# Performance work log

Hardware: AMD Instinct MI355X
Metric: run time of the kernel (lower is better)

The kernel has to match this reference:

```python
import jax, jax.numpy as jnp
import numpy as np
from jax import lax

B, T, I, H, C = 64, 512, 512, 1024, 1000


def _lstm_layer(x, W_ih, W_hh, b_ih, b_hh):
    # x: [B, T, in]; W_ih: [4H, in]; W_hh: [4H, H]; biases: [4H]
    # Precompute input projections for all timesteps (one big GEMM).
    xW = jnp.einsum('bti,gi->btg', x, W_ih) + b_ih + b_hh  # [B, T, 4H]
    h0 = jnp.zeros((x.shape[0], W_hh.shape[1]), x.dtype)
    c0 = jnp.zeros_like(h0)

    def step(carry, xw_t):
        h, c = carry
        gates = xw_t + h @ W_hh.T  # [B, 4H]
        i, f, g, o = jnp.split(gates, 4, axis=-1)  # PyTorch gate order i,f,g,o
        i = jax.nn.sigmoid(i)
        f = jax.nn.sigmoid(f)
        g = jnp.tanh(g)
        o = jax.nn.sigmoid(o)
        c = f * c + i * g
        h = o * jnp.tanh(c)
        return (h, c), h

    (h_T, c_T), hs = lax.scan(step, (h0, c0), jnp.swapaxes(xW, 0, 1))
    return jnp.swapaxes(hs, 0, 1), h_T  # [B, T, H], [B, H]


def setup_inputs() -> dict:
    key = jax.random.key(0)
    ks = jax.random.split(key, 11)
    s_i = 1.0 / np.sqrt(H)
    u = lambda k, shape: jax.random.uniform(k, shape, jnp.float32, -s_i, s_i)
    return {
        'x': jax.random.normal(ks[0], (B, T, I), jnp.float32),
        'W_ih0': u(ks[1], (4 * H, I)),
        'W_hh0': u(ks[2], (4 * H, H)),
        'b_ih0': u(ks[3], (4 * H,)),
        'b_hh0': u(ks[4], (4 * H,)),
        'W_ih1': u(ks[5], (4 * H, H)),
        'W_hh1': u(ks[6], (4 * H, H)),
        'b_ih1': u(ks[7], (4 * H,)),
        'b_hh1': u(ks[8], (4 * H,)),
        'W_d': u(ks[9], (C, H)),
        'b_d': u(ks[10], (C,)),
    }


def reference(x, W_ih0, W_hh0, b_ih0, b_hh0, W_ih1, W_hh1, b_ih1, b_hh1, W_d, b_d):
    h1_seq, _ = _lstm_layer(x, W_ih0, W_hh0, b_ih0, b_hh0)
    _, h_last = _lstm_layer(h1_seq, W_ih1, W_hh1, b_ih1, b_hh1)
    return h_last @ W_d.T + b_d  # [B, num_classes]
```

## Files before the change

### kernel.cpp

```cpp
#include <hip/hip_runtime.h>

typedef short short8 __attribute__((ext_vector_type(8)));
typedef float f32x4 __attribute__((ext_vector_type(4)));
typedef int i32x4 __attribute__((ext_vector_type(4)));
typedef unsigned short u16;
typedef unsigned long long u64;

#define NBLK 256
#define BDIM 512
#define BB 64
#define TT 512
#define II 512
#define HH 1024
#define NCLS 1000
#define HBUF (BB*HH)

__device__ __forceinline__ u16 f2bf(float f) {
  union { float f; unsigned u; } v; v.f = f;
  unsigned u = v.u;
  u += 0x7fffu + ((u >> 16) & 1u);
  return (u16)(u >> 16);
}

__device__ __forceinline__ short8 cvt8(f32x4 a, f32x4 b) {
  short8 v;
  v[0] = (short)f2bf(a[0]); v[1] = (short)f2bf(a[1]);
  v[2] = (short)f2bf(a[2]); v[3] = (short)f2bf(a[3]);
  v[4] = (short)f2bf(b[0]); v[5] = (short)f2bf(b[1]);
  v[6] = (short)f2bf(b[2]); v[7] = (short)f2bf(b[3]);
  return v;
}

__device__ __forceinline__ unsigned ld_rlx(const unsigned* p) {
  return __hip_atomic_load(p, __ATOMIC_RELAXED, __HIP_MEMORY_SCOPE_AGENT);
}
__device__ __forceinline__ void st_rlx(unsigned* p, unsigned v) {
  __hip_atomic_store(p, v, __ATOMIC_RELAXED, __HIP_MEMORY_SCOPE_AGENT);
}

__global__ void cvt_x(const float* __restrict__ x, u16* __restrict__ xb, int n8) {
  int i = blockIdx.x * blockDim.x + threadIdx.x;
  const int stride = gridDim.x * blockDim.x;
  for (; i < n8; i += stride) {
    f32x4 a = ((const f32x4*)x)[2 * i];
    f32x4 b = ((const f32x4*)x)[2 * i + 1];
    ((short8*)xb)[i] = cvt8(a, b);
  }
}

template<bool XBF>
__global__ __launch_bounds__(BDIM, 2) void lstm2_fused(
    const float* __restrict__ x, const u16* __restrict__ xb,
    const float* __restrict__ Wih0, const float* __restrict__ Whh0,
    const float* __restrict__ bih0, const float* __restrict__ bhh0,
    const float* __restrict__ Wih1, const float* __restrict__ Whh1,
    const float* __restrict__ bih1, const float* __restrict__ bhh1,
    u16* __restrict__ ring,
    u16* __restrict__ h1buf,
    float* __restrict__ h1f,
    unsigned* __restrict__ bar)
{
  __shared__ u16 wlds[32 * 2048];
  __shared__ float gbuf[64][33];
  __shared__ float blds[32];

  const bool isL1 = (blockIdx.x >= 128);
  const int wgl = isL1 ? (int)blockIdx.x - 128 : (int)blockIdx.x;
  const int j0 = wgl * 8;
  const int KX = isL1 ? HH : II;
  const int RL = KX + HH;
  const int ROWB = RL * 2;
  const float* Wih = isL1 ? Wih1 : Wih0;
  const float* Whh = isL1 ? Whh1 : Whh0;

  {
    const int cpr = RL / 8;
    for (int idx = threadIdx.x; idx < 32 * cpr; idx += BDIM) {
      int n = idx / cpr, cb = idx - n * cpr;
      int r = ((n >> 3) << 10) + j0 + (n & 7);
      int k = cb * 8;
      const float* src = (k < KX) ? (Wih + (size_t)r * KX + k)
                                  : (Whh + (size_t)r * HH + (k - KX));
      f32x4 a = *(const f32x4*)src;
      f32x4 b = *(const f32x4*)(src + 4);
      short8 v = cvt8(a, b);
      unsigned byte = (unsigned)(n * ROWB + k * 2) ^ ((unsigned)(n & 7) << 4);
      *(short8*)((char*)wlds + byte) = v;
    }
    if (threadIdx.x < 32) {
      int n = threadIdx.x;
      int r = ((n >> 3) << 10) + j0 + (n & 7);
      blds[n] = (isL1 ? bih1[r] : bih0[r]) + (isL1 ? bhh1[r] : bhh0[r]);
    }
  }
  __syncthreads();

  const int lane = threadIdx.x & 63;
  const int wid = threadIdx.x >> 6;
  const int mt = wid & 3, kg = wid >> 2;
  const int m0 = mt << 4;
  const int row_a = m0 + (lane & 15);
  const int koff = (lane >> 4) << 3;
  const unsigned mask = (unsigned)(lane & 7) << 4;
  const unsigned nb0 = (unsigned)((lane & 15) * ROWB);
  const unsigned nb1 = nb0 + (unsigned)(16 * ROWB);
  const char* wch = (const char*)wlds;

  const int tb = threadIdx.x >> 3, tj = threadIdx.x & 7;

  const int nsteps = RL >> 5;
  const int half = nsteps >> 1;
  const int ks_begin = kg * half, ks_end = ks_begin + half;
  const int bstep = KX >> 5;
  const int r1e = (ks_end < bstep) ? ks_end : bstep;
  const int r2b = (ks_begin > bstep) ? ks_begin : bstep;

  unsigned* const arrA = bar;
  unsigned* const relA = bar + 64;
  unsigned* const arrB = bar + 256;
  unsigned* const relB = bar + 320;

  float c_state = 0.f;

  auto kloop_h = [&](const u16* base, int kadj, int ks0, int ks1,
                     f32x4& A0, f32x4& A1) {
    for (int c = ks0; c < ks1; c += 8) {
      i32x4 av[8];
#pragma unroll
      for (int i = 0; i < 8; ++i) {
        const u16* p = base + (((c + i) << 5) + koff - kadj);
        asm volatile("global_load_dwordx4 %0, %1, off sc0 sc1"
                     : "=v"(av[i]) : "v"(p));
      }
      asm volatile("s_waitcnt vmcnt(0)" ::: "memory");
      __builtin_amdgcn_sched_barrier(0);
#pragma unroll
      for (int i = 0; i < 8; ++i) {
        int kk = ((c + i) << 5) + koff;
        unsigned o = (unsigned)(kk * 2) ^ mask;
        short8 bv0 = *(const short8*)(wch + (nb0 + o));
        short8 bv1 = *(const short8*)(wch + (nb1 + o));
        union { i32x4 q; short8 s; } u; u.q = av[i];
        A0 = __builtin_amdgcn_mfma_f32_16x16x32_bf16(u.s, bv0, A0, 0, 0, 0);
        A1 = __builtin_amdgcn_mfma_f32_16x16x32_bf16(u.s, bv1, A1, 0, 0, 0);
      }
    }
  };

  auto step_tail = [&](f32x4 acc0, f32x4 acc1, u16* hout, bool wf) {
    const int colA = lane & 15;
    const int rowD = m0 + ((lane >> 4) << 2);
    if (kg == 1) {
#pragma unroll
      for (int r = 0; r < 4; ++r) {
        gbuf[rowD + r][colA] = acc0[r];
        gbuf[rowD + r][colA + 16] = acc1[r];
      }
    }
    __syncthreads();
    if (kg == 0) {
#pragma unroll
      for (int r = 0; r < 4; ++r) {
        gbuf[rowD + r][colA] += acc0[r];
        gbuf[rowD + r][colA + 16] += acc1[r];
      }
    }
    __syncthreads();
    float gi = gbuf[tb][tj]      + blds[tj];
    float gf = gbuf[tb][8 + tj]  + blds[8 + tj];
    float gg = gbuf[tb][16 + tj] + blds[16 + tj];
    float go = gbuf[tb][24 + tj] + blds[24 + tj];
    gi = 1.f / (1.f + __expf(-gi));
    gf = 1.f / (1.f + __expf(-gf));
    go = 1.f / (1.f + __expf(-go));
    float e2 = __expf(2.f * fminf(15.f, fmaxf(-15.f, gg)));
    gg = (e2 - 1.f) / (e2 + 1.f);
    c_state = gf * c_state + gi * gg;
    float e2c = __expf(2.f * fminf(15.f, fmaxf(-15.f, c_state)));
    float th = (e2c - 1.f) / (e2c + 1.f);
    float hval = go * th;
    unsigned hu = (unsigned)f2bf(hval);
    unsigned nbv = (unsigned)__shfl_xor((int)hu, 1);
    if ((tj & 1) == 0) {
      unsigned packed = hu | (nbv << 16);
      unsigned* dst = (unsigned*)(hout + (size_t)tb * HH + j0 + tj);
      st_rlx(dst, packed);
    }
    if (wf) h1f[(size_t)tb * HH + j0 + tj] = hval;
  };

  if (!isL1) {
    for (int t = 0; t < TT; ++t) {
      if (t >= 3) {
        if (threadIdx.x == 0)
          while (ld_rlx(relB) < (unsigned)(t - 2)) __builtin_amdgcn_s_sleep(2);
        __syncthreads();
      }
      f32x4 acc0 = {0,0,0,0}, acc1 = {0,0,0,0};
      if (XBF) {
        const u16* xr = xb + (size_t)t * II + (size_t)row_a * ((size_t)TT * II);
#pragma unroll
        for (int ks = ks_begin; ks < r1e; ++ks) {
          int kk = (ks << 5) + koff;
          short8 av = *(const short8*)(xr + kk);
          unsigned o = (unsigned)(kk * 2) ^ mask;
          short8 bv0 = *(const short8*)(wch + (nb0 + o));
          short8 bv1 = *(const short8*)(wch + (nb1 + o));
          acc0 = __builtin_amdgcn_mfma_f32_16x16x32_bf16(av, bv0, acc0, 0, 0, 0);
          acc1 = __builtin_amdgcn_mfma_f32_16x16x32_bf16(av, bv1, acc1, 0, 0, 0);
        }
      } else {
        const float* xr = x + (size_t)t * II + (size_t)row_a * ((size_t)TT * II);
#pragma unroll
        for (int ks = ks_begin; ks < r1e; ++ks) {
          int kk = (ks << 5) + koff;
          short8 av = cvt8(*(const f32x4*)(xr + kk), *(const f32x4*)(xr + kk + 4));
          unsigned o = (unsigned)(kk * 2) ^ mask;
          short8 bv0 = *(const short8*)(wch + (nb0 + o));
          short8 bv1 = *(const short8*)(wch + (nb1 + o));
          acc0 = __builtin_amdgcn_mfma_f32_16x16x32_bf16(av, bv0, acc0, 0, 0, 0);
          acc1 = __builtin_amdgcn_mfma_f32_16x16x32_bf16(av, bv1, acc1, 0, 0, 0);
        }
      }
      kloop_h(ring + (size_t)((t + 2) % 3) * HBUF + (size_t)row_a * HH, KX,
              r2b, ks_end, acc0, acc1);
      step_tail(acc0, acc1, ring + (size_t)(t % 3) * HBUF, false);
      __syncthreads();
      if (threadIdx.x == 0) {
        unsigned old = atomicAdd(arrA, 1u);
        if (old == (unsigned)(128 * (t + 1) - 1)) st_rlx(relA, (unsigned)(t + 1));
        else if (t < TT - 1)
          while (ld_rlx(relA) < (unsigned)(t + 1)) __builtin_amdgcn_s_sleep(2);
      }
      __syncthreads();
    }
  } else {
    for (int t = 0; t < TT; ++t) {
      if (threadIdx.x == 0)
        while (ld_rlx(relA) < (unsigned)(t + 1)) __builtin_amdgcn_s_sleep(2);
      __syncthreads();
      f32x4 acc0 = {0,0,0,0}, acc1 = {0,0,0,0};
      kloop_h(ring + (size_t)(t % 3) * HBUF + (size_t)row_a * HH, 0,
              ks_begin, r1e, acc0, acc1);
      kloop_h(h1buf + (size_t)((t + 1) & 1) * HBUF + (size_t)row_a * HH, KX,
              r2b, ks_end, acc0, acc1);
      step_tail(acc0, acc1, h1buf + (size_t)(t & 1) * HBUF, t == TT - 1);
      if (t < TT - 1) {
        __syncthreads();
        if (threadIdx.x == 0) {
          unsigned old = atomicAdd(arrB, 1u);
          if (old == (unsigned)(128 * (t + 1) - 1)) st_rlx(relB, (unsigned)(t + 1));
          else
            while (ld_rlx(relB) < (unsigned)(t + 1)) __builtin_amdgcn_s_sleep(2);
        }
        __syncthreads();
      }
    }
  }
}

__global__ void dense_out(const float* __restrict__ h1, const float* __restrict__ Wd,
                          const float* __restrict__ bd, float* __restrict__ out)
{
  const int b  = threadIdx.x & 63;
  const int cl = threadIdx.x >> 6;
  const int cc = blockIdx.x * 4 + cl;
  float acc = 0.f;
  const float* hrow = h1 + (size_t)b * HH;
  const float* wrow = Wd + (size_t)cc * HH;
#pragma unroll 8
  for (int k = 0; k < HH; k += 4) {
    f32x4 hv = *(const f32x4*)(hrow + k);
    f32x4 wv = *(const f32x4*)(wrow + k);
    acc += hv[0] * wv[0] + hv[1] * wv[1] + hv[2] * wv[2] + hv[3] * wv[3];
  }
  out[(size_t)b * NCLS + cc] = acc + bd[cc];
}

extern "C" void kernel_launch(void* const* d_in, const int* in_sizes, int n_in,
                              void* d_out, int out_size, void* d_ws, size_t ws_size,
                              hipStream_t stream)
{
  (void)in_sizes; (void)n_in; (void)out_size;
  const float* x    = (const float*)d_in[0];
  const float* Wih0 = (const float*)d_in[1];
  const float* Whh0 = (const float*)d_in[2];
  const float* bih0 = (const float*)d_in[3];
  const float* bhh0 = (const float*)d_in[4];
  const float* Wih1 = (const float*)d_in[5];
  const float* Whh1 = (const float*)d_in[6];
  const float* bih1 = (const float*)d_in[7];
  const float* bhh1 = (const float*)d_in[8];
  const float* Wd   = (const float*)d_in[9];
  const float* bd   = (const float*)d_in[10];

  unsigned* bar = (unsigned*)d_ws;
  float* h1f  = (float*)((char*)d_ws + 4096);
  u16* h1buf  = (u16*)((char*)d_ws + 272 * 1024);
  u16* ring   = (u16*)((char*)d_ws + 528 * 1024);
  u16* xb     = (u16*)((char*)d_ws + (1u << 20));

  const size_t needA = (1u << 20) + (size_t)BB * TT * II * 2;
  const bool tierA = (ws_size >= needA);

  hipMemsetAsync(d_ws, 0, 912 * 1024, stream);

  if (tierA) {
    hipLaunchKernelGGL(cvt_x, dim3(2048), dim3(256), 0, stream,
                       x, xb, (int)((size_t)BB * TT * II / 8));
    hipLaunchKernelGGL((lstm2_fused<true>), dim3(NBLK), dim3(BDIM), 0, stream,
                       x, xb, Wih0, Whh0, bih0, bhh0, Wih1, Whh1, bih1, bhh1,
                       ring, h1buf, h1f, bar);
  } else {
    hipLaunchKernelGGL((lstm2_fused<false>), dim3(NBLK), dim3(BDIM), 0, stream,
                       x, xb, Wih0, Whh0, bih0, bhh0, Wih1, Whh1, bih1, bhh1,
                       ring, h1buf, h1f, bar);
  }
  hipLaunchKernelGGL(dense_out, dim3(250), dim3(256), 0, stream, h1f, Wd, bd,
                     (float*)d_out);
}
```

Measured before the change: 5.418 ms.

## Hold LSTM weights in registers and use 32x32 MFMA with 4-way K split

Each wave now preloads its slice of the recurrent and input weights from LDS into registers once, before the time loop, instead of re-reading them from LDS every step. The 16x16x32 MFMAs split two ways over K are replaced by 32x32x16 MFMAs split four ways over K, with each wave owning a 32-row batch half. The gate reduction now sums four partial buffers stored in the otherwise unused tail of the weight LDS region, which removes one barrier. This raises register pressure considerably (24 to 32 short8 values per lane) under launch bounds of 2 blocks, which may cause spills.

New measurement: 5.521 ms. Within noise of the previous version (+1.9%).

```diff
diff --git a/kernel.cpp b/kernel.cpp
--- a/kernel.cpp
+++ b/kernel.cpp
@@ -2,6 +2,7 @@
 
 typedef short short8 __attribute__((ext_vector_type(8)));
 typedef float f32x4 __attribute__((ext_vector_type(4)));
+typedef float f32x16 __attribute__((ext_vector_type(16)));
 typedef int i32x4 __attribute__((ext_vector_type(4)));
 typedef unsigned short u16;
 typedef unsigned long long u64;
@@ -45,6 +46,51 @@
     f32x4 a = ((const f32x4*)x)[2 * i];
     f32x4 b = ((const f32x4*)x)[2 * i + 1];
     ((short8*)xb)[i] = cvt8(a, b);
+  }
+}
+
+
+template<int N, int B0, int MH>
+__device__ __forceinline__ void run_coh(const u16* lanep,
+                                        const short8 (&breg)[MH], f32x16& acc) {
+  static_assert(N % 8 == 0, "");
+#pragma unroll
+  for (int c = 0; c < N; c += 8) {
+    i32x4 av[8];
+#pragma unroll
+    for (int i = 0; i < 8; ++i) {
+      const u16* p = lanep + (c + i) * 16;
+      asm volatile("global_load_dwordx4 %0, %1, off sc0 sc1"
+                   : "=v"(av[i]) : "v"(p));
+    }
+    asm volatile("s_waitcnt vmcnt(0)" ::: "memory");
+    __builtin_amdgcn_sched_barrier(0);
+#pragma unroll
+    for (int i = 0; i < 8; ++i) {
+      union { i32x4 q; short8 s; } u; u.q = av[i];
+      acc = __builtin_amdgcn_mfma_f32_32x32x16_bf16(u.s, breg[B0 + c + i], acc, 0, 0, 0);
+    }
+  }
+}
+
+template<int N, int B0, int MH>
+__device__ __forceinline__ void run_pb(const u16* lanep,
+                                       const short8 (&breg)[MH], f32x16& acc) {
+#pragma unroll
+  for (int i = 0; i < N; ++i) {
+    short8 av = *(const short8*)(lanep + i * 16);
+    acc = __builtin_amdgcn_mfma_f32_32x32x16_bf16(av, breg[B0 + i], acc, 0, 0, 0);
+  }
+}
+
+template<int N, int B0, int MH>
+__device__ __forceinline__ void run_pf(const float* lanep,
+                                       const short8 (&breg)[MH], f32x16& acc) {
+#pragma unroll
+  for (int i = 0; i < N; ++i) {
+    short8 av = cvt8(*(const f32x4*)(lanep + i * 16),
+                     *(const f32x4*)(lanep + i * 16 + 4));
+    acc = __builtin_amdgcn_mfma_f32_32x32x16_bf16(av, breg[B0 + i], acc, 0, 0, 0);
   }
 }
 
@@ -61,8 +107,8 @@
     unsigned* __restrict__ bar)
 {
   __shared__ u16 wlds[32 * 2048];
-  __shared__ float gbuf[64][33];
   __shared__ float blds[32];
+  float (*g4)[64][32] = (float(*)[64][32])((char*)wlds + 98304);
 
   const bool isL1 = (blockIdx.x >= 128);
   const int wgl = isL1 ? (int)blockIdx.x - 128 : (int)blockIdx.x;
@@ -97,23 +143,12 @@
 
   const int lane = threadIdx.x & 63;
   const int wid = threadIdx.x >> 6;
-  const int mt = wid & 3, kg = wid >> 2;
-  const int m0 = mt << 4;
-  const int row_a = m0 + (lane & 15);
-  const int koff = (lane >> 4) << 3;
-  const unsigned mask = (unsigned)(lane & 7) << 4;
-  const unsigned nb0 = (unsigned)((lane & 15) * ROWB);
-  const unsigned nb1 = nb0 + (unsigned)(16 * ROWB);
+  const int mp = wid & 1, kq = wid >> 1;
+  const int row_a = mp * 32 + (lane & 31);
+  const int sub8 = (lane >> 5) << 3;
   const char* wch = (const char*)wlds;
 
   const int tb = threadIdx.x >> 3, tj = threadIdx.x & 7;
-
-  const int nsteps = RL >> 5;
-  const int half = nsteps >> 1;
-  const int ks_begin = kg * half, ks_end = ks_begin + half;
-  const int bstep = KX >> 5;
-  const int r1e = (ks_end < bstep) ? ks_end : bstep;
-  const int r2b = (ks_begin > bstep) ? ks_begin : bstep;
 
   unsigned* const arrA = bar;
   unsigned* const relA = bar + 64;
@@ -122,59 +157,25 @@
 
   float c_state = 0.f;
 
-  auto kloop_h = [&](const u16* base, int kadj, int ks0, int ks1,
-                     f32x4& A0, f32x4& A1) {
-    for (int c = ks0; c < ks1; c += 8) {
-      i32x4 av[8];
-#pragma unroll
-      for (int i = 0; i < 8; ++i) {
-        const u16* p = base + (((c + i) << 5) + koff - kadj);
-        asm volatile("global_load_dwordx4 %0, %1, off sc0 sc1"
-                     : "=v"(av[i]) : "v"(p));
-      }
-      asm volatile("s_waitcnt vmcnt(0)" ::: "memory");
-      __builtin_amdgcn_sched_barrier(0);
-#pragma unroll
-      for (int i = 0; i < 8; ++i) {
-        int kk = ((c + i) << 5) + koff;
-        unsigned o = (unsigned)(kk * 2) ^ mask;
-        short8 bv0 = *(const short8*)(wch + (nb0 + o));
-        short8 bv1 = *(const short8*)(wch + (nb1 + o));
-        union { i32x4 q; short8 s; } u; u.q = av[i];
-        A0 = __builtin_amdgcn_mfma_f32_16x16x32_bf16(u.s, bv0, A0, 0, 0, 0);
-        A1 = __builtin_amdgcn_mfma_f32_16x16x32_bf16(u.s, bv1, A1, 0, 0, 0);
-      }
-    }
-  };
-
-  auto step_tail = [&](f32x4 acc0, f32x4 acc1, u16* hout, bool wf) {
-    const int colA = lane & 15;
-    const int rowD = m0 + ((lane >> 4) << 2);
-    if (kg == 1) {
-#pragma unroll
-      for (int r = 0; r < 4; ++r) {
-        gbuf[rowD + r][colA] = acc0[r];
-        gbuf[rowD + r][colA + 16] = acc1[r];
-      }
+  auto step_tail = [&](const f32x16& acc, u16* hout, bool wf) {
+    const int col = lane & 31;
+    const int rbase = mp * 32 + ((lane >> 5) << 2);
+#pragma unroll
+    for (int r = 0; r < 16; ++r) {
+      int brow = rbase + (r & 3) + ((r >> 2) << 3);
+      g4[kq][brow][col] = acc[r];
     }
     __syncthreads();
-    if (kg == 0) {
-#pragma unroll
-      for (int r = 0; r < 4; ++r) {
-        gbuf[rowD + r][colA] += acc0[r];
-        gbuf[rowD + r][colA + 16] += acc1[r];
-      }
-    }
-    __syncthreads();
-    float gi = gbuf[tb][tj]      + blds[tj];
-    float gf = gbuf[tb][8 + tj]  + blds[8 + tj];
-    float gg = gbuf[tb][16 + tj] + blds[16 + tj];
-    float go = gbuf[tb][24 + tj] + blds[24 + tj];
-    gi = 1.f / (1.f + __expf(-gi));
-    gf = 1.f / (1.f + __expf(-gf));
-    go = 1.f / (1.f + __expf(-go));
-    float e2 = __expf(2.f * fminf(15.f, fmaxf(-15.f, gg)));
-    gg = (e2 - 1.f) / (e2 + 1.f);
+    float gv[4];
+#pragma unroll
+    for (int g = 0; g < 4; ++g)
+      gv[g] = g4[0][tb][g * 8 + tj] + g4[1][tb][g * 8 + tj]
+            + g4[2][tb][g * 8 + tj] + g4[3][tb][g * 8 + tj] + blds[g * 8 + tj];
+    float gi = 1.f / (1.f + __expf(-gv[0]));
+    float gf = 1.f / (1.f + __expf(-gv[1]));
+    float e2 = __expf(2.f * fminf(15.f, fmaxf(-15.f, gv[2])));
+    float gg = (e2 - 1.f) / (e2 + 1.f);
+    float go = 1.f / (1.f + __expf(-gv[3]));
     c_state = gf * c_state + gi * gg;
     float e2c = __expf(2.f * fminf(15.f, fmaxf(-15.f, c_state)));
     float th = (e2c - 1.f) / (e2c + 1.f);
@@ -190,41 +191,42 @@
   };
 
   if (!isL1) {
+    short8 breg[24];
+#pragma unroll
+    for (int i = 0; i < 24; ++i) {
+      int k = (kq * 24 + i) * 16 + sub8;
+      unsigned byte = ((unsigned)((lane & 31) * ROWB + k * 2))
+                      ^ ((unsigned)(lane & 7) << 4);
+      breg[i] = *(const short8*)(wch + byte);
+    }
+    __syncthreads();
+
     for (int t = 0; t < TT; ++t) {
       if (t >= 3) {
         if (threadIdx.x == 0)
           while (ld_rlx(relB) < (unsigned)(t - 2)) __builtin_amdgcn_s_sleep(2);
         __syncthreads();
       }
-      f32x4 acc0 = {0,0,0,0}, acc1 = {0,0,0,0};
+      f32x16 acc = {};
+      const u16* hb = ring + (size_t)((t + 2) % 3) * HBUF + (size_t)row_a * HH;
       if (XBF) {
-        const u16* xr = xb + (size_t)t * II + (size_t)row_a * ((size_t)TT * II);
-#pragma unroll
-        for (int ks = ks_begin; ks < r1e; ++ks) {
-          int kk = (ks << 5) + koff;
-          short8 av = *(const short8*)(xr + kk);
-          unsigned o = (unsigned)(kk * 2) ^ mask;
-          short8 bv0 = *(const short8*)(wch + (nb0 + o));
-          short8 bv1 = *(const short8*)(wch + (nb1 + o));
-          acc0 = __builtin_amdgcn_mfma_f32_16x16x32_bf16(av, bv0, acc0, 0, 0, 0);
-          acc1 = __builtin_amdgcn_mfma_f32_16x16x32_bf16(av, bv1, acc1, 0, 0, 0);
-        }
+        const u16* xl = xb + (size_t)t * II + (size_t)row_a * ((size_t)TT * II)
+                        + kq * 384 + sub8;
+        if (kq == 0)      run_pb<24, 0>(xl, breg, acc);
+        else if (kq == 1) { run_pb<8, 0>(xl, breg, acc);
+                            run_coh<16, 8>(hb + 0 + sub8, breg, acc); }
+        else if (kq == 2) run_coh<24, 0>(hb + 256 + sub8, breg, acc);
+        else              run_coh<24, 0>(hb + 640 + sub8, breg, acc);
       } else {
-        const float* xr = x + (size_t)t * II + (size_t)row_a * ((size_t)TT * II);
-#pragma unroll
-        for (int ks = ks_begin; ks < r1e; ++ks) {
-          int kk = (ks << 5) + koff;
-          short8 av = cvt8(*(const f32x4*)(xr + kk), *(const f32x4*)(xr + kk + 4));
-          unsigned o = (unsigned)(kk * 2) ^ mask;
-          short8 bv0 = *(const short8*)(wch + (nb0 + o));
-          short8 bv1 = *(const short8*)(wch + (nb1 + o));
-          acc0 = __builtin_amdgcn_mfma_f32_16x16x32_bf16(av, bv0, acc0, 0, 0, 0);
-          acc1 = __builtin_amdgcn_mfma_f32_16x16x32_bf16(av, bv1, acc1, 0, 0, 0);
-        }
+        const float* xl = x + (size_t)t * II + (size_t)row_a * ((size_t)TT * II)
+                          + kq * 384 + sub8;
+        if (kq == 0)      run_pf<24, 0>(xl, breg, acc);
+        else if (kq == 1) { run_pf<8, 0>(xl, breg, acc);
+                            run_coh<16, 8>(hb + 0 + sub8, breg, acc); }
+        else if (kq == 2) run_coh<24, 0>(hb + 256 + sub8, breg, acc);
+        else              run_coh<24, 0>(hb + 640 + sub8, breg, acc);
       }
-      kloop_h(ring + (size_t)((t + 2) % 3) * HBUF + (size_t)row_a * HH, KX,
-              r2b, ks_end, acc0, acc1);
-      step_tail(acc0, acc1, ring + (size_t)(t % 3) * HBUF, false);
+      step_tail(acc, ring + (size_t)(t % 3) * HBUF, false);
       __syncthreads();
       if (threadIdx.x == 0) {
         unsigned old = atomicAdd(arrA, 1u);
@@ -235,16 +237,29 @@
       __syncthreads();
     }
   } else {
+    short8 breg[32];
+#pragma unroll
+    for (int i = 0; i < 32; ++i) {
+      int k = (kq * 32 + i) * 16 + sub8;
+      unsigned byte = ((unsigned)((lane & 31) * ROWB + k * 2))
+                      ^ ((unsigned)(lane & 7) << 4);
+      breg[i] = *(const short8*)(wch + byte);
+    }
+    __syncthreads();
+
     for (int t = 0; t < TT; ++t) {
       if (threadIdx.x == 0)
         while (ld_rlx(relA) < (unsigned)(t + 1)) __builtin_amdgcn_s_sleep(2);
       __syncthreads();
-      f32x4 acc0 = {0,0,0,0}, acc1 = {0,0,0,0};
-      kloop_h(ring + (size_t)(t % 3) * HBUF + (size_t)row_a * HH, 0,
-              ks_begin, r1e, acc0, acc1);
-      kloop_h(h1buf + (size_t)((t + 1) & 1) * HBUF + (size_t)row_a * HH, KX,
-              r2b, ks_end, acc0, acc1);
-      step_tail(acc0, acc1, h1buf + (size_t)(t & 1) * HBUF, t == TT - 1);
+      f32x16 acc = {};
+      const u16* lp;
+      if (kq < 2)
+        lp = ring + (size_t)(t % 3) * HBUF + (size_t)row_a * HH + kq * 512 + sub8;
+      else
+        lp = h1buf + (size_t)((t + 1) & 1) * HBUF + (size_t)row_a * HH
+             + (kq - 2) * 512 + sub8;
+      run_coh<32, 0>(lp, breg, acc);
+      step_tail(acc, h1buf + (size_t)(t & 1) * HBUF, t == TT - 1);
       if (t < TT - 1) {
         __syncthreads();
         if (threadIdx.x == 0) {
```
